# Performance work log

Measured on AMD Instinct MI355X. Metric: run time of the kernel, lower is better.

The kernel has to match this reference:

```python
import jax, jax.numpy as jnp
import numpy as np

HID = 3584
NH = 28
NKV = 4
HD = HID // NH  # 128
T = 2048
THETA = 1000000.0
SCALE = HD ** -0.5


def setup_inputs() -> dict:
    key = jax.random.key(0)
    ks = jax.random.split(key, 9)
    s = 0.02
    return {
        "positions": jnp.arange(T, dtype=jnp.int32),
        "hidden_states": jax.random.normal(ks[0], (T, HID), dtype=jnp.float32),
        "wq": jax.random.normal(ks[1], (HID, NH * HD), dtype=jnp.float32) * s,
        "bq": jax.random.normal(ks[2], (NH * HD,), dtype=jnp.float32) * s,
        "wk": jax.random.normal(ks[3], (HID, NKV * HD), dtype=jnp.float32) * s,
        "bk": jax.random.normal(ks[4], (NKV * HD,), dtype=jnp.float32) * s,
        "wv": jax.random.normal(ks[5], (HID, NKV * HD), dtype=jnp.float32) * s,
        "bv": jax.random.normal(ks[6], (NKV * HD,), dtype=jnp.float32) * s,
        "wo": jax.random.normal(ks[7], (NH * HD, HID), dtype=jnp.float32) * s,
    }


def _rope(x, positions):
    # neox-style RoPE over full head_dim: split halves, rotate.
    half = HD // 2
    inv_freq = 1.0 / (THETA ** (jnp.arange(0, half, dtype=jnp.float32) / half))
    ang = positions.astype(jnp.float32)[:, None] * inv_freq  # [T, half]
    cos = jnp.cos(ang)[:, None, :]  # [T, 1, half]
    sin = jnp.sin(ang)[:, None, :]
    x1, x2 = x[..., :half], x[..., half:]
    return jnp.concatenate([x1 * cos - x2 * sin, x2 * cos + x1 * sin], axis=-1)


def reference(positions, hidden_states, wq, bq, wk, bk, wv, bv, wo):
    q = (hidden_states @ wq + bq).reshape(T, NH, HD)
    k = (hidden_states @ wk + bk).reshape(T, NKV, HD)
    v = (hidden_states @ wv + bv).reshape(T, NKV, HD)
    q = _rope(q, positions)
    k = _rope(k, positions)
    # GQA: expand kv heads to query heads (groups of NH//NKV)
    g = NH // NKV
    k = jnp.repeat(k, g, axis=1)  # [T, NH, HD]
    v = jnp.repeat(v, g, axis=1)
    scores = jnp.einsum("thd,shd->hts", q, k) * SCALE  # bidirectional, no mask
    probs = jax.nn.softmax(scores, axis=-1)
    attn = jnp.einsum("hts,shd->thd", probs, v).reshape(T, NH * HD)
    return attn @ wo
```

## Files before the change

kernel.cpp:

```cpp
#include <hip/hip_runtime.h>

typedef __bf16 bf16_t;
typedef __attribute__((ext_vector_type(8))) __bf16 bf16x8;
typedef __attribute__((ext_vector_type(4))) float floatx4;

#define T_SEQ 2048
#define HID 3584
#define NH 28
#define NKV 4
#define HD 128
#define GQA 7
#define SCALE_F 0.08838834764831845f
#define QSCALE_LOG2 0.1275179100693744f

__global__ void conv_bf_k(const float* __restrict__ src, bf16_t* __restrict__ dst, long n) {
  const long i = ((long)blockIdx.x * 256 + threadIdx.x) * 8;
  if (i >= n) return;
  const floatx4 a = *(const floatx4*)(src + i);
  const floatx4 b = *(const floatx4*)(src + i + 4);
  bf16x8 r;
  r[0] = (bf16_t)a[0]; r[1] = (bf16_t)a[1]; r[2] = (bf16_t)a[2]; r[3] = (bf16_t)a[3];
  r[4] = (bf16_t)b[0]; r[5] = (bf16_t)b[1]; r[6] = (bf16_t)b[2]; r[7] = (bf16_t)b[3];
  *(bf16x8*)(dst + i) = r;
}

__global__ __launch_bounds__(256) void tconv_k(const float* __restrict__ src,
                                               bf16_t* __restrict__ dst, long N, long K) {
  __shared__ alignas(16) bf16_t t[64][72];
  const long k0 = (long)blockIdx.y * 64, n0 = (long)blockIdx.x * 64;
  const int tid = threadIdx.x;
  const int rr = tid >> 4;
  const int cc = (tid & 15) * 4;
#pragma unroll
  for (int i = 0; i < 4; ++i) {
    const int r = rr + i * 16;
    const floatx4 v = *(const floatx4*)(src + (k0 + r) * N + n0 + cc);
#pragma unroll
    for (int j = 0; j < 4; ++j) t[cc + j][r] = (bf16_t)v[j];
  }
  __syncthreads();
#pragma unroll
  for (int i = 0; i < 2; ++i) {
    const int J = i * 256 + tid;
    const int n = J >> 3, c8 = (J & 7) * 8;
    *(bf16x8*)(dst + (n0 + n) * K + k0 + c8) = *(const bf16x8*)(&t[n][c8]);
  }
}

__device__ __forceinline__ bf16x8 ld8(const void* p, long idx, bool f32) {
  if (f32) {
    const float* q = (const float*)p + idx;
    const floatx4 u = *(const floatx4*)q;
    const floatx4 v = *(const floatx4*)(q + 4);
    bf16x8 r;
    r[0] = (bf16_t)u[0]; r[1] = (bf16_t)u[1]; r[2] = (bf16_t)u[2]; r[3] = (bf16_t)u[3];
    r[4] = (bf16_t)v[0]; r[5] = (bf16_t)v[1]; r[6] = (bf16_t)v[2]; r[7] = (bf16_t)v[3];
    return r;
  }
  return *(const bf16x8*)((const bf16_t*)p + idx);
}

__device__ __forceinline__ void gld16(const bf16_t* g, bf16_t* l) {
  __builtin_amdgcn_global_load_lds(
      (const __attribute__((address_space(1))) unsigned int*)(const void*)g,
      (__attribute__((address_space(3))) unsigned int*)(void*)l, 16, 0, 0);
}

__global__ __launch_bounds__(256) void gemm_bt_k(
    const bf16_t* __restrict__ A, long lda,
    const bf16_t* __restrict__ Bt, long ldb,
    const float* __restrict__ bias, void* Cv, long ldc,
    int K, int mode) {
  __shared__ alignas(16) bf16_t ldsA[128 * 32];
  __shared__ alignas(16) bf16_t ldsB[128 * 32];
  const int tid = threadIdx.x;
  const int lane = tid & 63;
  const int w = tid >> 6;
  const int wr = w >> 1, wc = w & 1;
  const int col = lane & 15, quad = lane >> 4;
  const long m0 = (long)blockIdx.y * 128, n0 = (long)blockIdx.x * 128;

  const int r0 = tid >> 2, ch = (tid & 3) * 8;
  const int r1 = 64 + r0;

  floatx4 acc[4][4] = {};

  for (int k0 = 0; k0 < K; k0 += 32) {
    gld16(A + (m0 + r0) * lda + k0 + ch, ldsA + tid * 8);
    gld16(A + (m0 + r1) * lda + k0 + ch, ldsA + (256 + tid) * 8);
    gld16(Bt + (n0 + r0) * ldb + k0 + ch, ldsB + tid * 8);
    gld16(Bt + (n0 + r1) * ldb + k0 + ch, ldsB + (256 + tid) * 8);
    __syncthreads();
    bf16x8 af[4], bf[4];
#pragma unroll
    for (int i = 0; i < 4; ++i)
      af[i] = *(const bf16x8*)(ldsA + (wr * 64 + i * 16 + col) * 32 + quad * 8);
#pragma unroll
    for (int j = 0; j < 4; ++j)
      bf[j] = *(const bf16x8*)(ldsB + (wc * 64 + j * 16 + col) * 32 + quad * 8);
#pragma unroll
    for (int i = 0; i < 4; ++i)
#pragma unroll
      for (int j = 0; j < 4; ++j)
        acc[i][j] = __builtin_amdgcn_mfma_f32_16x16x32_bf16(af[i], bf[j], acc[i][j], 0, 0, 0);
    __syncthreads();
  }

#pragma unroll
  for (int i = 0; i < 4; ++i) {
#pragma unroll
    for (int j = 0; j < 4; ++j) {
      const long row0 = m0 + wr * 64 + i * 16 + quad * 4;
      const long cc = n0 + wc * 64 + j * 16 + col;
      const float bvv = bias ? bias[cc] : 0.f;
#pragma unroll
      for (int r = 0; r < 4; ++r) {
        const float v = acc[i][j][r] + bvv;
        if (mode == 0)      ((bf16_t*)Cv)[(row0 + r) * ldc + cc] = (bf16_t)v;
        else if (mode == 1) ((float*)Cv)[(row0 + r) * ldc + cc] = v;
        else {
          if (cc < 512) ((bf16_t*)Cv)[(row0 + r) * 512 + cc] = (bf16_t)v;
          else ((bf16_t*)Cv)[1048576 + (cc - 512) * (long)T_SEQ + (row0 + r)] = (bf16_t)v;
        }
      }
    }
  }
}

__global__ __launch_bounds__(256) void gemm_nt_k(
    const void* A, long lda, const void* B, long ldb,
    const float* bias, void* Cv, long ldc,
    int K, int aMode, int bMode, int transC, int c32, const int* flag) {
  __shared__ alignas(16) bf16_t ldsA[128 * 32];
  __shared__ alignas(16) unsigned int ldsB32[128 * 16];
  const int f = *flag;
  const bool aF32 = aMode && (f > 32);
  const bool bF32 = bMode && (f > 32);
  const int tid = threadIdx.x;
  const int lane = tid & 63;
  const int w = tid >> 6;
  const int wr = w >> 1, wc = w & 1;
  const int col = lane & 15, quad = lane >> 4;
  const long m0 = (long)blockIdx.y * 128, n0 = (long)blockIdx.x * 128;

  const int ar1 = tid >> 2, ak = (tid & 3) * 8;
  const int ar2 = 64 + ar1;
  const int kk = (tid >> 4) * 2;
  const int nn = (tid & 15) * 8;
  const int kp = kk >> 1;

  floatx4 acc[4][4] = {};

  for (int k0 = 0; k0 < K; k0 += 32) {
    const bf16x8 a1 = ld8(A, (m0 + ar1) * lda + k0 + ak, aF32);
    const bf16x8 a2 = ld8(A, (m0 + ar2) * lda + k0 + ak, aF32);
    const bf16x8 b0 = ld8(B, (long)(k0 + kk) * ldb + n0 + nn, bF32);
    const bf16x8 b1 = ld8(B, (long)(k0 + kk + 1) * ldb + n0 + nn, bF32);
    __syncthreads();
    *(bf16x8*)(ldsA + ar1 * 32 + ak) = a1;
    *(bf16x8*)(ldsA + ar2 * 32 + ak) = a2;
#pragma unroll
    for (int j = 0; j < 8; ++j) {
      const int n = nn + j;
      const int pk = ((((kp >> 2) ^ ((n >> 3) & 3)) << 2) | (kp & 3));
      union { struct { bf16_t lo, hi; } s; unsigned int u; } cv;
      cv.s.lo = b0[j];
      cv.s.hi = b1[j];
      ldsB32[n * 16 + pk] = cv.u;
    }
    __syncthreads();
    bf16x8 af[4], bfv[4];
#pragma unroll
    for (int i = 0; i < 4; ++i)
      af[i] = *(const bf16x8*)(ldsA + (wr * 64 + i * 16 + col) * 32 + quad * 8);
#pragma unroll
    for (int j = 0; j < 4; ++j) {
      const int n = wc * 64 + j * 16 + col;
      const int blk = quad ^ ((n >> 3) & 3);
      bfv[j] = *(const bf16x8*)((const bf16_t*)(ldsB32 + n * 16 + blk * 4));
    }
#pragma unroll
    for (int i = 0; i < 4; ++i)
#pragma unroll
      for (int jj = 0; jj < 4; ++jj)
        acc[i][jj] = __builtin_amdgcn_mfma_f32_16x16x32_bf16(af[i], bfv[jj], acc[i][jj], 0, 0, 0);
  }

#pragma unroll
  for (int i = 0; i < 4; ++i) {
#pragma unroll
    for (int j = 0; j < 4; ++j) {
      const long row0 = m0 + wr * 64 + i * 16 + quad * 4;
      const long cc = n0 + wc * 64 + j * 16 + col;
      const float bvv = bias ? bias[cc] : 0.f;
#pragma unroll
      for (int r = 0; r < 4; ++r) {
        const float v = acc[i][j][r] + bvv;
        if (transC)   ((bf16_t*)Cv)[cc * ldc + (row0 + r)] = (bf16_t)v;
        else if (c32) ((float*)Cv)[(row0 + r) * ldc + cc] = v;
        else          ((bf16_t*)Cv)[(row0 + r) * ldc + cc] = (bf16_t)v;
      }
    }
  }
}

__global__ void rope_k(bf16_t* buf, const int* __restrict__ pos, long ld, int nheads) {
  const int idx = blockIdx.x * 256 + threadIdx.x;
  const int total = T_SEQ * nheads * 64;
  if (idx >= total) return;
  const int d = idx & 63;
  const int th = idx >> 6;
  const int h = th % nheads;
  const int t = th / nheads;
  const float inv = exp2f((float)d * (-19.931568569324174f / 64.f));
  const float ang = (float)pos[t] * inv;
  float sn, cs;
  __sincosf(ang, &sn, &cs);
  bf16_t* p = buf + (long)t * ld + h * HD + d;
  const float x1 = (float)p[0];
  const float x2 = (float)p[64];
  p[0] = (bf16_t)(x1 * cs - x2 * sn);
  p[64] = (bf16_t)(x2 * cs + x1 * sn);
}

__global__ __launch_bounds__(512) void attn4_k(
    const bf16_t* __restrict__ q, long qs,
    const bf16_t* __restrict__ k, long ks,
    const bf16_t* __restrict__ vt,
    bf16_t* __restrict__ out, long os) {
  __shared__ alignas(16) bf16_t ldsK[2][64 * 128];
  __shared__ alignas(16) bf16_t ldsV[2][128 * 64];
  __shared__ alignas(16) bf16_t pbuf[8][16 * 64];

  const int h = blockIdx.y;
  const long hkvHD = (long)(h / GQA) * HD;
  const int tid = threadIdx.x;
  const int lane = tid & 63;
  const int w = tid >> 6;
  const int col = lane & 15, quad = lane >> 4;
  const int t0 = blockIdx.x * 128 + w * 16;

  auto stage = [&](int buf, int t) {
    const long s0 = (long)t * 64;
#pragma unroll
    for (int i = 0; i < 2; ++i) {
      const int J = i * 512 + tid;
      {
        const int row = J >> 4;
        const int cs = (J & 15) ^ (row & 7);
        gld16(k + (s0 + row) * ks + hkvHD + cs * 8, &ldsK[buf][J * 8]);
      }
      {
        const int row = J >> 3;
        const int cs = (J & 7) ^ (row & 7);
        gld16(vt + (hkvHD + row) * T_SEQ + s0 + cs * 8, &ldsV[buf][J * 8]);
      }
    }
  };

  bf16x8 aq[4];
  {
    const bf16_t* qp = q + (long)(t0 + col) * qs + h * HD + quad * 8;
#pragma unroll
    for (int c = 0; c < 4; ++c) {
      aq[c] = *(const bf16x8*)(qp + c * 32);
#pragma unroll
      for (int e = 0; e < 8; ++e) aq[c][e] = (bf16_t)((float)aq[c][e] * QSCALE_LOG2);
    }
  }

  bf16x8 ones;
#pragma unroll
  for (int e = 0; e < 8; ++e) ones[e] = (bf16_t)1.0f;

  floatx4 O[8] = {};
  float m_w = -1e30f;
  float l_i[4];
#pragma unroll
  for (int r = 0; r < 4; ++r) l_i[r] = 0.f;

  stage(0, 0);
  for (int t = 0; t < 32; ++t) {
    const int cur = t & 1;
    stage(cur ^ 1, (t + 1) & 31);
    __builtin_amdgcn_sched_barrier(0);
    asm volatile("s_waitcnt vmcnt(4)" ::: "memory");
    __builtin_amdgcn_sched_barrier(0);
    __builtin_amdgcn_s_barrier();
    __builtin_amdgcn_sched_barrier(0);

    floatx4 S[4] = {};
    __builtin_amdgcn_s_setprio(1);
#pragma unroll
    for (int nt = 0; nt < 4; ++nt) {
      const int row = nt * 16 + col;
#pragma unroll
      for (int c = 0; c < 4; ++c) {
        const int cs = (c * 4 + quad) ^ (row & 7);
        const bf16x8 bk = *(const bf16x8*)(&ldsK[cur][row * 128 + cs * 8]);
        S[nt] = __builtin_amdgcn_mfma_f32_16x16x32_bf16(aq[c], bk, S[nt], 0, 0, 0);
      }
    }
    __builtin_amdgcn_s_setprio(0);

    float mx = S[0][0];
#pragma unroll
    for (int nt = 0; nt < 4; ++nt)
#pragma unroll
      for (int r = 0; r < 4; ++r) mx = fmaxf(mx, S[nt][r]);
#pragma unroll
    for (int off = 1; off < 64; off <<= 1)
      mx = fmaxf(mx, __shfl_xor(mx, off, 64));

    if (mx > m_w + 12.0f) {
      const float alpha = exp2f(m_w - mx);
      m_w = mx;
#pragma unroll
      for (int r = 0; r < 4; ++r) l_i[r] *= alpha;
#pragma unroll
      for (int dt = 0; dt < 8; ++dt)
#pragma unroll
        for (int r = 0; r < 4; ++r) O[dt][r] *= alpha;
    }

#pragma unroll
    for (int r = 0; r < 4; ++r) {
      const int mrow = quad * 4 + r;
#pragma unroll
      for (int nt = 0; nt < 4; ++nt) {
        const float p = exp2f(S[nt][r] - m_w);
        const int cs = (nt * 2 + (col >> 3)) ^ (mrow & 7);
        pbuf[w][mrow * 64 + cs * 8 + (col & 7)] = (bf16_t)p;
      }
    }

    floatx4 Ssum = {};
    __builtin_amdgcn_s_setprio(1);
#pragma unroll
    for (int kb = 0; kb < 2; ++kb) {
      const int csp = (kb * 4 + quad) ^ (col & 7);
      const bf16x8 pa = *(const bf16x8*)(&pbuf[w][col * 64 + csp * 8]);
      Ssum = __builtin_amdgcn_mfma_f32_16x16x32_bf16(pa, ones, Ssum, 0, 0, 0);
#pragma unroll
      for (int dt = 0; dt < 8; ++dt) {
        const int vrow = dt * 16 + col;
        const bf16x8 bv = *(const bf16x8*)(&ldsV[cur][vrow * 64 + csp * 8]);
        O[dt] = __builtin_amdgcn_mfma_f32_16x16x32_bf16(pa, bv, O[dt], 0, 0, 0);
      }
    }
    __builtin_amdgcn_s_setprio(0);
#pragma unroll
    for (int r = 0; r < 4; ++r) l_i[r] += Ssum[r];

    __builtin_amdgcn_sched_barrier(0);
    __builtin_amdgcn_s_barrier();
    __builtin_amdgcn_sched_barrier(0);
  }

#pragma unroll
  for (int r = 0; r < 4; ++r) l_i[r] = 1.f / l_i[r];
#pragma unroll
  for (int dt = 0; dt < 8; ++dt) {
#pragma unroll
    for (int r = 0; r < 4; ++r) {
      const long trow = t0 + quad * 4 + r;
      out[trow * os + h * HD + dt * 16 + col] = (bf16_t)(O[dt][r] * l_i[r]);
    }
  }
}

extern "C" void kernel_launch(void* const* d_in, const int* in_sizes, int n_in,
                              void* d_out_v, int out_size, void* d_ws, size_t ws_size,
                              hipStream_t stream) {
  const int* pos = (const int*)d_in[0];
  const float* hidden = (const float*)d_in[1];
  const float* wq = (const float*)d_in[2];
  const float* bq = (const float*)d_in[3];
  const float* wk = (const float*)d_in[4];
  const float* bk = (const float*)d_in[5];
  const float* wv = (const float*)d_in[6];
  const float* bv = (const float*)d_in[7];
  const float* wo = (const float*)d_in[8];

  bf16_t* qbuf = (bf16_t*)d_out_v;
  bf16_t* attn_hi = (bf16_t*)d_out_v + (size_t)T_SEQ * HID;
  float* outf = (float*)d_out_v;

  char* ws = (char*)d_ws;
  const size_t NEED = 51904516;

  if (ws_size >= NEED) {
    bf16_t* hbf  = (bf16_t*)ws;
    bf16_t* wqbt = (bf16_t*)(ws + 14680064);
    bf16_t* wkbt = (bf16_t*)(ws + 40370176);
    bf16_t* wvbt = (bf16_t*)(ws + 44040192);
    bf16_t* kbuf = (bf16_t*)(ws + 47710208);
    bf16_t* vt   = (bf16_t*)(ws + 49807360);
    bf16_t* wobt = wqbt;
    bf16_t* attnb = hbf;
    float* bkv = (float*)attn_hi;

    hipMemcpyAsync(bkv, bk, 512 * sizeof(float), hipMemcpyDeviceToDevice, stream);
    hipMemcpyAsync(bkv + 512, bv, 512 * sizeof(float), hipMemcpyDeviceToDevice, stream);

    conv_bf_k<<<3584, 256, 0, stream>>>(hidden, hbf, (long)T_SEQ * HID);
    tconv_k<<<dim3(56, 56), 256, 0, stream>>>(wq, wqbt, HID, HID);
    tconv_k<<<dim3(8, 56), 256, 0, stream>>>(wk, wkbt, 512, HID);
    tconv_k<<<dim3(8, 56), 256, 0, stream>>>(wv, wvbt, 512, HID);

    gemm_bt_k<<<dim3(28, 16), 256, 0, stream>>>(hbf, HID, wqbt, HID, bq, qbuf, HID,
                                                HID, 0);
    gemm_bt_k<<<dim3(8, 16), 256, 0, stream>>>(hbf, HID, wkbt, HID, bkv, kbuf, 512,
                                               HID, 2);

    rope_k<<<(T_SEQ * NH * 64) / 256, 256, 0, stream>>>(qbuf, pos, HID, NH);
    rope_k<<<(T_SEQ * NKV * 64) / 256, 256, 0, stream>>>(kbuf, pos, 512, NKV);

    attn4_k<<<dim3(16, 28), 512, 0, stream>>>(qbuf, HID, kbuf, 512, vt, attnb, HID);

    tconv_k<<<dim3(56, 56), 256, 0, stream>>>(wo, wobt, HID, HID);

    gemm_bt_k<<<dim3(28, 16), 256, 0, stream>>>(attnb, HID, wobt, HID, nullptr,
                                                outf, HID, HID, 1);
  } else {
    bf16_t* kbuf = (bf16_t*)ws;
    bf16_t* vt = (bf16_t*)(ws + 2097152);
    bf16_t* acopy = (bf16_t*)ws;
    int* flag = (int*)(ws + 4194304);

    hipMemsetAsync(flag, 64, 4, stream);

    gemm_nt_k<<<dim3(28, 16), 256, 0, stream>>>(hidden, HID, wq, HID, bq, qbuf, HID,
                                                HID, 1, 1, 0, 0, flag);
    gemm_nt_k<<<dim3(4, 16), 256, 0, stream>>>(hidden, HID, wk, 512, bk, kbuf, 512,
                                               HID, 1, 1, 0, 0, flag);
    gemm_nt_k<<<dim3(4, 16), 256, 0, stream>>>(hidden, HID, wv, 512, bv, vt, T_SEQ,
                                               HID, 1, 1, 1, 0, flag);

    rope_k<<<(T_SEQ * NH * 64) / 256, 256, 0, stream>>>(qbuf, pos, HID, NH);
    rope_k<<<(T_SEQ * NKV * 64) / 256, 256, 0, stream>>>(kbuf, pos, 512, NKV);

    attn4_k<<<dim3(16, 28), 512, 0, stream>>>(qbuf, HID, kbuf, 512, vt, attn_hi, HID);

    hipMemcpyAsync(acopy, attn_hi + (size_t)1536 * HID, (size_t)512 * HID * 2,
                   hipMemcpyDeviceToDevice, stream);
    gemm_nt_k<<<dim3(28, 8), 256, 0, stream>>>(attn_hi, HID, wo, HID, nullptr,
                                               outf, HID, HID, 0, 1, 0, 1, flag);
    gemm_nt_k<<<dim3(28, 4), 256, 0, stream>>>(attn_hi + (size_t)1024 * HID, HID, wo, HID,
                                               nullptr, outf + (size_t)1024 * HID, HID,
                                               HID, 0, 1, 0, 1, flag);
    gemm_nt_k<<<dim3(28, 4), 256, 0, stream>>>(acopy, HID, wo, HID,
                                               nullptr, outf + (size_t)1536 * HID, HID,
                                               HID, 0, 1, 0, 1, flag);
  }
}
```

Measured before the change: 584.0 us.

## Fuse QKV projections into one GEMM and give each attention wave 32 query rows

The Q and K/V projection GEMMs become a single launch over the contiguous transposed wq/wk/wv buffers with one concatenated bias. A new epilogue mode routes Q columns, K columns and transposed V columns to their separate outputs. The attention kernel moves from 8 waves of 16 query rows to 4 waves of 32 rows, so each K and V fragment read from LDS feeds two MFMA tiles. This halves LDS fragment reads per query row and removes one GEMM launch and its tail. In exchange it raises register pressure in the attention kernel (twice the accumulators and softmax state) and halves the threads per block that stage K/V tiles.

```diff
diff --git a/kernel.cpp b/kernel.cpp
--- a/kernel.cpp
+++ b/kernel.cpp
@@ -70,7 +70,7 @@
     const bf16_t* __restrict__ A, long lda,
     const bf16_t* __restrict__ Bt, long ldb,
     const float* __restrict__ bias, void* Cv, long ldc,
-    int K, int mode) {
+    int K, int mode, void* Cv2) {
   __shared__ alignas(16) bf16_t ldsA[128 * 32];
   __shared__ alignas(16) bf16_t ldsB[128 * 32];
   const int tid = threadIdx.x;
@@ -119,8 +119,9 @@
         if (mode == 0)      ((bf16_t*)Cv)[(row0 + r) * ldc + cc] = (bf16_t)v;
         else if (mode == 1) ((float*)Cv)[(row0 + r) * ldc + cc] = v;
         else {
-          if (cc < 512) ((bf16_t*)Cv)[(row0 + r) * 512 + cc] = (bf16_t)v;
-          else ((bf16_t*)Cv)[1048576 + (cc - 512) * (long)T_SEQ + (row0 + r)] = (bf16_t)v;
+          if (cc < 3584)      ((bf16_t*)Cv)[(row0 + r) * ldc + cc] = (bf16_t)v;
+          else if (cc < 4096) ((bf16_t*)Cv2)[(row0 + r) * 512 + (cc - 3584)] = (bf16_t)v;
+          else ((bf16_t*)Cv2)[1048576 + (cc - 4096) * (long)T_SEQ + (row0 + r)] = (bf16_t)v;
         }
       }
     }
@@ -223,14 +224,14 @@
   p[64] = (bf16_t)(x2 * cs + x1 * sn);
 }
 
-__global__ __launch_bounds__(512) void attn4_k(
+__global__ __launch_bounds__(256, 2) void attn5_k(
     const bf16_t* __restrict__ q, long qs,
     const bf16_t* __restrict__ k, long ks,
     const bf16_t* __restrict__ vt,
     bf16_t* __restrict__ out, long os) {
   __shared__ alignas(16) bf16_t ldsK[2][64 * 128];
   __shared__ alignas(16) bf16_t ldsV[2][128 * 64];
-  __shared__ alignas(16) bf16_t pbuf[8][16 * 64];
+  __shared__ alignas(16) bf16_t pbuf[4][32 * 64];
 
   const int h = blockIdx.y;
   const long hkvHD = (long)(h / GQA) * HD;
@@ -238,13 +239,13 @@
   const int lane = tid & 63;
   const int w = tid >> 6;
   const int col = lane & 15, quad = lane >> 4;
-  const int t0 = blockIdx.x * 128 + w * 16;
+  const int t0 = blockIdx.x * 128 + w * 32;
 
   auto stage = [&](int buf, int t) {
     const long s0 = (long)t * 64;
 #pragma unroll
-    for (int i = 0; i < 2; ++i) {
-      const int J = i * 512 + tid;
+    for (int i = 0; i < 4; ++i) {
+      const int J = i * 256 + tid;
       {
         const int row = J >> 4;
         const int cs = (J & 15) ^ (row & 7);
@@ -258,14 +259,16 @@
     }
   };
 
-  bf16x8 aq[4];
-  {
-    const bf16_t* qp = q + (long)(t0 + col) * qs + h * HD + quad * 8;
+  bf16x8 aq[2][4];
+#pragma unroll
+  for (int sub = 0; sub < 2; ++sub) {
+    const bf16_t* qp = q + (long)(t0 + sub * 16 + col) * qs + h * HD + quad * 8;
 #pragma unroll
     for (int c = 0; c < 4; ++c) {
-      aq[c] = *(const bf16x8*)(qp + c * 32);
-#pragma unroll
-      for (int e = 0; e < 8; ++e) aq[c][e] = (bf16_t)((float)aq[c][e] * QSCALE_LOG2);
+      aq[sub][c] = *(const bf16x8*)(qp + c * 32);
+#pragma unroll
+      for (int e = 0; e < 8; ++e)
+        aq[sub][c][e] = (bf16_t)((float)aq[sub][c][e] * QSCALE_LOG2);
     }
   }
 
@@ -273,23 +276,21 @@
 #pragma unroll
   for (int e = 0; e < 8; ++e) ones[e] = (bf16_t)1.0f;
 
-  floatx4 O[8] = {};
-  float m_w = -1e30f;
-  float l_i[4];
-#pragma unroll
-  for (int r = 0; r < 4; ++r) l_i[r] = 0.f;
+  floatx4 O[2][8] = {};
+  float m_w[2] = {-1e30f, -1e30f};
+  float l_i[2][4] = {};
 
   stage(0, 0);
   for (int t = 0; t < 32; ++t) {
     const int cur = t & 1;
     stage(cur ^ 1, (t + 1) & 31);
     __builtin_amdgcn_sched_barrier(0);
-    asm volatile("s_waitcnt vmcnt(4)" ::: "memory");
+    asm volatile("s_waitcnt vmcnt(8)" ::: "memory");
     __builtin_amdgcn_sched_barrier(0);
     __builtin_amdgcn_s_barrier();
     __builtin_amdgcn_sched_barrier(0);
 
-    floatx4 S[4] = {};
+    floatx4 S[2][4] = {};
     __builtin_amdgcn_s_setprio(1);
 #pragma unroll
     for (int nt = 0; nt < 4; ++nt) {
@@ -298,59 +299,69 @@
       for (int c = 0; c < 4; ++c) {
         const int cs = (c * 4 + quad) ^ (row & 7);
         const bf16x8 bk = *(const bf16x8*)(&ldsK[cur][row * 128 + cs * 8]);
-        S[nt] = __builtin_amdgcn_mfma_f32_16x16x32_bf16(aq[c], bk, S[nt], 0, 0, 0);
+        S[0][nt] = __builtin_amdgcn_mfma_f32_16x16x32_bf16(aq[0][c], bk, S[0][nt], 0, 0, 0);
+        S[1][nt] = __builtin_amdgcn_mfma_f32_16x16x32_bf16(aq[1][c], bk, S[1][nt], 0, 0, 0);
       }
     }
     __builtin_amdgcn_s_setprio(0);
 
-    float mx = S[0][0];
-#pragma unroll
-    for (int nt = 0; nt < 4; ++nt)
-#pragma unroll
-      for (int r = 0; r < 4; ++r) mx = fmaxf(mx, S[nt][r]);
-#pragma unroll
-    for (int off = 1; off < 64; off <<= 1)
-      mx = fmaxf(mx, __shfl_xor(mx, off, 64));
-
-    if (mx > m_w + 12.0f) {
-      const float alpha = exp2f(m_w - mx);
-      m_w = mx;
-#pragma unroll
-      for (int r = 0; r < 4; ++r) l_i[r] *= alpha;
-#pragma unroll
-      for (int dt = 0; dt < 8; ++dt)
-#pragma unroll
-        for (int r = 0; r < 4; ++r) O[dt][r] *= alpha;
-    }
-
-#pragma unroll
-    for (int r = 0; r < 4; ++r) {
-      const int mrow = quad * 4 + r;
-#pragma unroll
-      for (int nt = 0; nt < 4; ++nt) {
-        const float p = exp2f(S[nt][r] - m_w);
-        const int cs = (nt * 2 + (col >> 3)) ^ (mrow & 7);
-        pbuf[w][mrow * 64 + cs * 8 + (col & 7)] = (bf16_t)p;
-      }
-    }
-
-    floatx4 Ssum = {};
+#pragma unroll
+    for (int sub = 0; sub < 2; ++sub) {
+      float mx = S[sub][0][0];
+#pragma unroll
+      for (int nt = 0; nt < 4; ++nt)
+#pragma unroll
+        for (int r = 0; r < 4; ++r) mx = fmaxf(mx, S[sub][nt][r]);
+#pragma unroll
+      for (int off = 1; off < 64; off <<= 1)
+        mx = fmaxf(mx, __shfl_xor(mx, off, 64));
+      if (mx > m_w[sub] + 12.0f) {
+        const float alpha = exp2f(m_w[sub] - mx);
+        m_w[sub] = mx;
+#pragma unroll
+        for (int r = 0; r < 4; ++r) l_i[sub][r] *= alpha;
+#pragma unroll
+        for (int dt = 0; dt < 8; ++dt)
+#pragma unroll
+          for (int r = 0; r < 4; ++r) O[sub][dt][r] *= alpha;
+      }
+    }
+
+#pragma unroll
+    for (int sub = 0; sub < 2; ++sub)
+#pragma unroll
+      for (int r = 0; r < 4; ++r) {
+        const int mrow = sub * 16 + quad * 4 + r;
+#pragma unroll
+        for (int nt = 0; nt < 4; ++nt) {
+          const float p = exp2f(S[sub][nt][r] - m_w[sub]);
+          const int cs = (nt * 2 + (col >> 3)) ^ (mrow & 7);
+          pbuf[w][mrow * 64 + cs * 8 + (col & 7)] = (bf16_t)p;
+        }
+      }
+
+    floatx4 Ssum[2] = {};
     __builtin_amdgcn_s_setprio(1);
 #pragma unroll
     for (int kb = 0; kb < 2; ++kb) {
       const int csp = (kb * 4 + quad) ^ (col & 7);
-      const bf16x8 pa = *(const bf16x8*)(&pbuf[w][col * 64 + csp * 8]);
-      Ssum = __builtin_amdgcn_mfma_f32_16x16x32_bf16(pa, ones, Ssum, 0, 0, 0);
+      const bf16x8 pa0 = *(const bf16x8*)(&pbuf[w][(col) * 64 + csp * 8]);
+      const bf16x8 pa1 = *(const bf16x8*)(&pbuf[w][(16 + col) * 64 + csp * 8]);
+      Ssum[0] = __builtin_amdgcn_mfma_f32_16x16x32_bf16(pa0, ones, Ssum[0], 0, 0, 0);
+      Ssum[1] = __builtin_amdgcn_mfma_f32_16x16x32_bf16(pa1, ones, Ssum[1], 0, 0, 0);
 #pragma unroll
       for (int dt = 0; dt < 8; ++dt) {
         const int vrow = dt * 16 + col;
         const bf16x8 bv = *(const bf16x8*)(&ldsV[cur][vrow * 64 + csp * 8]);
-        O[dt] = __builtin_amdgcn_mfma_f32_16x16x32_bf16(pa, bv, O[dt], 0, 0, 0);
+        O[0][dt] = __builtin_amdgcn_mfma_f32_16x16x32_bf16(pa0, bv, O[0][dt], 0, 0, 0);
+        O[1][dt] = __builtin_amdgcn_mfma_f32_16x16x32_bf16(pa1, bv, O[1][dt], 0, 0, 0);
       }
     }
     __builtin_amdgcn_s_setprio(0);
 #pragma unroll
-    for (int r = 0; r < 4; ++r) l_i[r] += Ssum[r];
+    for (int sub = 0; sub < 2; ++sub)
+#pragma unroll
+      for (int r = 0; r < 4; ++r) l_i[sub][r] += Ssum[sub][r];
 
     __builtin_amdgcn_sched_barrier(0);
     __builtin_amdgcn_s_barrier();
@@ -358,13 +369,16 @@
   }
 
 #pragma unroll
-  for (int r = 0; r < 4; ++r) l_i[r] = 1.f / l_i[r];
-#pragma unroll
-  for (int dt = 0; dt < 8; ++dt) {
-#pragma unroll
-    for (int r = 0; r < 4; ++r) {
-      const long trow = t0 + quad * 4 + r;
-      out[trow * os + h * HD + dt * 16 + col] = (bf16_t)(O[dt][r] * l_i[r]);
+  for (int sub = 0; sub < 2; ++sub) {
+#pragma unroll
+    for (int r = 0; r < 4; ++r) l_i[sub][r] = 1.f / l_i[sub][r];
+#pragma unroll
+    for (int dt = 0; dt < 8; ++dt) {
+#pragma unroll
+      for (int r = 0; r < 4; ++r) {
+        const long trow = t0 + sub * 16 + quad * 4 + r;
+        out[trow * os + h * HD + dt * 16 + col] = (bf16_t)(O[sub][dt][r] * l_i[sub][r]);
+      }
     }
   }
 }
@@ -398,30 +412,29 @@
     bf16_t* vt   = (bf16_t*)(ws + 49807360);
     bf16_t* wobt = wqbt;
     bf16_t* attnb = hbf;
-    float* bkv = (float*)attn_hi;
-
-    hipMemcpyAsync(bkv, bk, 512 * sizeof(float), hipMemcpyDeviceToDevice, stream);
-    hipMemcpyAsync(bkv + 512, bv, 512 * sizeof(float), hipMemcpyDeviceToDevice, stream);
+    float* bqkv = (float*)attn_hi;
+
+    hipMemcpyAsync(bqkv, bq, 3584 * sizeof(float), hipMemcpyDeviceToDevice, stream);
+    hipMemcpyAsync(bqkv + 3584, bk, 512 * sizeof(float), hipMemcpyDeviceToDevice, stream);
+    hipMemcpyAsync(bqkv + 4096, bv, 512 * sizeof(float), hipMemcpyDeviceToDevice, stream);
 
     conv_bf_k<<<3584, 256, 0, stream>>>(hidden, hbf, (long)T_SEQ * HID);
     tconv_k<<<dim3(56, 56), 256, 0, stream>>>(wq, wqbt, HID, HID);
     tconv_k<<<dim3(8, 56), 256, 0, stream>>>(wk, wkbt, 512, HID);
     tconv_k<<<dim3(8, 56), 256, 0, stream>>>(wv, wvbt, 512, HID);
 
-    gemm_bt_k<<<dim3(28, 16), 256, 0, stream>>>(hbf, HID, wqbt, HID, bq, qbuf, HID,
-                                                HID, 0);
-    gemm_bt_k<<<dim3(8, 16), 256, 0, stream>>>(hbf, HID, wkbt, HID, bkv, kbuf, 512,
-                                               HID, 2);
+    gemm_bt_k<<<dim3(36, 16), 256, 0, stream>>>(hbf, HID, wqbt, HID, bqkv, qbuf, HID,
+                                                HID, 3, kbuf);
 
     rope_k<<<(T_SEQ * NH * 64) / 256, 256, 0, stream>>>(qbuf, pos, HID, NH);
     rope_k<<<(T_SEQ * NKV * 64) / 256, 256, 0, stream>>>(kbuf, pos, 512, NKV);
 
-    attn4_k<<<dim3(16, 28), 512, 0, stream>>>(qbuf, HID, kbuf, 512, vt, attnb, HID);
+    attn5_k<<<dim3(16, 28), 256, 0, stream>>>(qbuf, HID, kbuf, 512, vt, attnb, HID);
 
     tconv_k<<<dim3(56, 56), 256, 0, stream>>>(wo, wobt, HID, HID);
 
     gemm_bt_k<<<dim3(28, 16), 256, 0, stream>>>(attnb, HID, wobt, HID, nullptr,
-                                                outf, HID, HID, 1);
+                                                outf, HID, HID, 1, nullptr);
   } else {
     bf16_t* kbuf = (bf16_t*)ws;
     bf16_t* vt = (bf16_t*)(ws + 2097152);
@@ -440,7 +453,7 @@
     rope_k<<<(T_SEQ * NH * 64) / 256, 256, 0, stream>>>(qbuf, pos, HID, NH);
     rope_k<<<(T_SEQ * NKV * 64) / 256, 256, 0, stream>>>(kbuf, pos, 512, NKV);
 
-    attn4_k<<<dim3(16, 28), 512, 0, stream>>>(qbuf, HID, kbuf, 512, vt, attn_hi, HID);
+    attn5_k<<<dim3(16, 28), 256, 0, stream>>>(qbuf, HID, kbuf, 512, vt, attn_hi, HID);
 
     hipMemcpyAsync(acopy, attn_hi + (size_t)1536 * HID, (size_t)512 * HID * 2,
                    hipMemcpyDeviceToDevice, stream);
```

Measured after the change: 527.7 us. 9.6% less time.
